# Performance work log

Hardware: AMD Instinct MI355X
Metric: run time of the kernel (lower is better)

Reference implementation:

```python
import jax, jax.numpy as jnp
import numpy as np

B, S, D, H = 4, 2048, 1024, 16
HD = D // H


def setup_inputs() -> dict:
    key = jax.random.key(0)
    ks = jax.random.split(key, 12)
    scale = 1.0 / np.sqrt(D)
    inp = {
        "query": jax.random.normal(ks[0], (B, S, D), jnp.float32),
        "key_": jax.random.normal(ks[1], (B, S, D), jnp.float32),
        "value": jax.random.normal(ks[2], (B, S, D), jnp.float32),
        "Wq": jax.random.normal(ks[3], (D, D), jnp.float32) * scale,
        "bq": jnp.zeros((D,), jnp.float32),
        "Wk": jax.random.normal(ks[4], (D, D), jnp.float32) * scale,
        "bk": jnp.zeros((D,), jnp.float32),
        "Wv": jax.random.normal(ks[5], (D, D), jnp.float32) * scale,
        "bv": jnp.zeros((D,), jnp.float32),
        "Wo": jax.random.normal(ks[6], (D, D), jnp.float32) * scale,
        "bo": jnp.zeros((D,), jnp.float32),
        # causal mask: 1 where attention allowed, 0 where masked (masked_fill(mask==0, -inf))
        "mask": jnp.tril(jnp.ones((S, S), jnp.int32))[None, None, :, :],
    }
    return inp


def reference(query, key_, value, Wq, bq, Wk, bk, Wv, bv, Wo, bo, mask):
    def split_heads(x):  # [B,S,D] -> [B,H,S,HD]
        return x.reshape(B, S, H, HD).transpose(0, 2, 1, 3)

    Q = split_heads(query @ Wq.T + bq)
    K = split_heads(key_ @ Wk.T + bk)
    V = split_heads(value @ Wv.T + bv)

    scores = jnp.einsum("bhqd,bhkd->bhqk", Q, K) / np.sqrt(HD).astype(np.float32)
    scores = jnp.where(mask == 0, -jnp.inf, scores)
    attn = jax.nn.softmax(scores, axis=-1)  # [B,H,S,S]
    out = jnp.einsum("bhqk,bhkd->bhqd", attn, V)  # [B,H,S,HD]
    concat = out.transpose(0, 2, 1, 3).reshape(B, S, D)
    return concat @ Wo.T + bo
```

## Files before the change

kernel.cpp:

```cpp
#include <hip/hip_runtime.h>
#include <hip/hip_bf16.h>
#include <math.h>

#define BB 4
#define SS 2048
#define DD 1024
#define HH 16
#define HD 64

#define NEG_BIG (-1e30f)


typedef short v8s __attribute__((ext_vector_type(8)));
typedef float v4f __attribute__((ext_vector_type(4)));

__device__ inline unsigned cvt_pk_bf16(float lo, float hi) {
    unsigned r;
    asm("v_cvt_pk_bf16_f32 %0, %1, %2" : "=v"(r) : "v"(lo), "v"(hi));
    return r;
}

__device__ inline short f2bf(float f) {
    return (short)cvt_pk_bf16(f, f);
}

__device__ inline v4f v4f_zero() {
    v4f z;
    z[0] = 0.f; z[1] = 0.f; z[2] = 0.f; z[3] = 0.f;
    return z;
}

__device__ inline v8s load8f(const float* p) {
    v4f a = *(const v4f*)p;
    v4f b = *(const v4f*)(p + 4);
    union { unsigned u[4]; v8s s; } x;
    x.u[0] = cvt_pk_bf16(a[0], a[1]);
    x.u[1] = cvt_pk_bf16(a[2], a[3]);
    x.u[2] = cvt_pk_bf16(b[0], b[1]);
    x.u[3] = cvt_pk_bf16(b[2], b[3]);
    return x.s;
}

template <int MODE>
__global__ __launch_bounds__(256) void gemm_bt_kernel(
    const void* __restrict__ Av, const float* __restrict__ Bm,
    const float* __restrict__ bias, void* __restrict__ Cv,
    int M, int N, int K) {
    __shared__ short sA[128 * 32];
    __shared__ short sB[128 * 32];

    const int tid = threadIdx.x;
    const int lane = tid & 63;
    const int wave = tid >> 6;
    const int quad = lane >> 4;
    const int l16 = lane & 15;
    const int wm = wave >> 1;
    const int wn = wave & 1;
    const int m0 = blockIdx.y * 128;
    const int n0 = blockIdx.x * 128;

    v4f acc[4][4];
#pragma unroll
    for (int i = 0; i < 4; i++)
#pragma unroll
        for (int j = 0; j < 4; j++) acc[i][j] = v4f_zero();

    for (int k0 = 0; k0 < K; k0 += 32) {
        __syncthreads();
#pragma unroll
        for (int p = 0; p < 2; p++) {
            int idx = (p * 256 + tid) * 8;
            int r = idx >> 5;
            int c = idx & 31;
            if (MODE == 3) {
                int m = m0 + r;
                int k = k0 + c;
                int b = m >> 11, s = m & 2047, h = k >> 6, d = k & 63;
                *(v8s*)&sA[idx] = *(const v8s*)&(
                    (const short*)Av)[(((size_t)(b * HH + h) * SS + s) << 6) + d];
            } else {
                *(v8s*)&sA[idx] =
                    load8f((const float*)Av + (size_t)(m0 + r) * K + k0 + c);
            }
            *(v8s*)&sB[idx] = load8f(Bm + (size_t)(n0 + r) * K + k0 + c);
        }
        __syncthreads();

        v8s af[4], bfr[4];
#pragma unroll
        for (int i = 0; i < 4; i++)
            af[i] = *(const v8s*)&sA[(wm * 64 + i * 16 + l16) * 32 + quad * 8];
#pragma unroll
        for (int j = 0; j < 4; j++)
            bfr[j] = *(const v8s*)&sB[(wn * 64 + j * 16 + l16) * 32 + quad * 8];
#pragma unroll
        for (int i = 0; i < 4; i++)
#pragma unroll
            for (int j = 0; j < 4; j++)
                acc[i][j] = __builtin_amdgcn_mfma_f32_16x16x32_bf16(
                    af[i], bfr[j], acc[i][j], 0, 0, 0);
    }

#pragma unroll
    for (int i = 0; i < 4; i++) {
#pragma unroll
        for (int j = 0; j < 4; j++) {
#pragma unroll
            for (int r = 0; r < 4; r++) {
                int ml = wm * 64 + i * 16 + quad * 4 + r;
                int nl = wn * 64 + j * 16 + l16;
                int m = m0 + ml;
                int n = n0 + nl;
                float v = acc[i][j][r];
                if (MODE == 0) {
                    v += bias[n];
                    int b = m >> 11, s = m & 2047, h = n >> 6, d = n & 63;
                    ((short*)Cv)[(((size_t)(b * HH + h) * SS + s) << 6) + d] =
                        f2bf(v);
                } else if (MODE == 1) {
                    v += bias[m];
                    int h = m >> 6, d = m & 63, b = n >> 11, s = n & 2047;
                    ((short*)Cv)[((size_t)(b * HH + h) * HD + d) * SS + s] =
                        f2bf(v);
                } else {
                    v += bias[n];
                    ((float*)Cv)[(size_t)m * N + n] = v;
                }
            }
        }
    }
}

__global__ __launch_bounds__(256) void attn_kernel(
    short* __restrict__ QO, const short* __restrict__ Kt,
    const short* __restrict__ Vt) {
    constexpr int LDR = 64 + 8;
    __shared__ short sK[64 * LDR];
    __shared__ short sV[64 * LDR];
    __shared__ short sP[4][16 * LDR];

    const int tid = threadIdx.x;
    const int lane = tid & 63;
    const int wave = tid >> 6;
    const int quad = lane >> 4;
    const int l16 = lane & 15;
    const int qt = (int)gridDim.x - 1 - (int)blockIdx.x;
    const int bh = blockIdx.y;

    short* Qh = QO + (size_t)bh * SS * HD;
    const short* Kh = Kt + (size_t)bh * SS * HD;
    const short* Vh = Vt + (size_t)bh * HD * SS;

    const int qrow = qt * 64 + wave * 16 + l16;
    v8s qf[2];
    qf[0] = *(const v8s*)&Qh[(size_t)qrow * HD + quad * 8];
    qf[1] = *(const v8s*)&Qh[(size_t)qrow * HD + 32 + quad * 8];

    v8s onesb;
#pragma unroll
    for (int i = 0; i < 8; i++) onesb[i] = (short)0x3F80;

    v4f o[4];
#pragma unroll
    for (int j = 0; j < 4; j++) o[j] = v4f_zero();
    v4f oSum = v4f_zero();
    float mOld[4];
#pragma unroll
    for (int r = 0; r < 4; r++) mOld[r] = NEG_BIG;

    const int qg_base = qt * 64 + wave * 16 + quad * 4;

    for (int kt = 0; kt <= qt; kt++) {
        __syncthreads();
#pragma unroll
        for (int p = 0; p < 2; p++) {
            int idx = (p * 256 + tid) * 8;
            int r = idx >> 6;
            int c = idx & 63;
            *(v8s*)&sK[r * LDR + c] =
                *(const v8s*)&Kh[(size_t)(kt * 64 + r) * HD + c];
            *(v8s*)&sV[r * LDR + c] =
                *(const v8s*)&Vh[(size_t)r * SS + kt * 64 + c];
        }
        __syncthreads();

        __builtin_amdgcn_s_setprio(1);
        v4f sc[4];
#pragma unroll
        for (int j = 0; j < 4; j++) {
            v8s b0 = *(const v8s*)&sK[(j * 16 + l16) * LDR + quad * 8];
            v8s b1 = *(const v8s*)&sK[(j * 16 + l16) * LDR + 32 + quad * 8];
            v4f t = __builtin_amdgcn_mfma_f32_16x16x32_bf16(qf[0], b0,
                                                            v4f_zero(), 0, 0, 0);
            sc[j] = __builtin_amdgcn_mfma_f32_16x16x32_bf16(qf[1], b1, t, 0, 0, 0);
        }
        __builtin_amdgcn_s_setprio(0);

        float x[4][4];
        const bool diag = (kt == qt);
#pragma unroll
        for (int j = 0; j < 4; j++) {
#pragma unroll
            for (int r = 0; r < 4; r++) {
                float v = sc[j][r] * 0.125f;
                if (diag) {
                    int kg = kt * 64 + j * 16 + l16;
                    int qg = qg_base + r;
                    if (kg > qg) v = NEG_BIG;
                }
                x[j][r] = v;
            }
        }

        float mNew[4], alpha[4];
#pragma unroll
        for (int r = 0; r < 4; r++) {
            float t = fmaxf(fmaxf(x[0][r], x[1][r]), fmaxf(x[2][r], x[3][r]));
#pragma unroll
            for (int off = 8; off >= 1; off >>= 1) t = fmaxf(t, __shfl_xor(t, off));
            mNew[r] = fmaxf(mOld[r], t);
            alpha[r] = __expf(mOld[r] - mNew[r]);
            mOld[r] = mNew[r];
        }

        short* Pw = sP[wave];
#pragma unroll
        for (int j = 0; j < 4; j++)
#pragma unroll
            for (int r = 0; r < 4; r++) {
                float p = __expf(x[j][r] - mNew[r]);
                Pw[(quad * 4 + r) * LDR + j * 16 + l16] = f2bf(p);
            }
#pragma unroll
        for (int j = 0; j < 4; j++)
#pragma unroll
            for (int r = 0; r < 4; r++) o[j][r] *= alpha[r];
#pragma unroll
        for (int r = 0; r < 4; r++) oSum[r] *= alpha[r];


        v8s pa0 = *(const v8s*)&Pw[l16 * LDR + quad * 8];
        v8s pa1 = *(const v8s*)&Pw[l16 * LDR + 32 + quad * 8];
        __builtin_amdgcn_s_setprio(1);
#pragma unroll
        for (int j = 0; j < 4; j++) {
            v8s v0 = *(const v8s*)&sV[(j * 16 + l16) * LDR + quad * 8];
            v8s v1 = *(const v8s*)&sV[(j * 16 + l16) * LDR + 32 + quad * 8];
            o[j] = __builtin_amdgcn_mfma_f32_16x16x32_bf16(pa0, v0, o[j], 0, 0, 0);
            o[j] = __builtin_amdgcn_mfma_f32_16x16x32_bf16(pa1, v1, o[j], 0, 0, 0);
        }
        oSum = __builtin_amdgcn_mfma_f32_16x16x32_bf16(pa0, onesb, oSum, 0, 0, 0);
        oSum = __builtin_amdgcn_mfma_f32_16x16x32_bf16(pa1, onesb, oSum, 0, 0, 0);
        __builtin_amdgcn_s_setprio(0);
    }

#pragma unroll
    for (int r = 0; r < 4; r++) {
        float inv = 1.f / oSum[r];
        int s = qg_base + r;
#pragma unroll
        for (int j = 0; j < 4; j++) {
            float v = o[j][r] * inv;
            Qh[(size_t)s * HD + j * 16 + l16] = f2bf(v);
        }
    }
}

extern "C" void kernel_launch(void* const* d_in, const int* in_sizes, int n_in,
                              void* d_out, int out_size, void* d_ws, size_t ws_size,
                              hipStream_t stream) {
    const float* query = (const float*)d_in[0];
    const float* key_ = (const float*)d_in[1];
    const float* value = (const float*)d_in[2];
    const float* Wq = (const float*)d_in[3];
    const float* bq = (const float*)d_in[4];
    const float* Wk = (const float*)d_in[5];
    const float* bk = (const float*)d_in[6];
    const float* Wv = (const float*)d_in[7];
    const float* bv = (const float*)d_in[8];
    const float* Wo = (const float*)d_in[9];
    const float* bo = (const float*)d_in[10];
    float* out = (float*)d_out;

    const size_t NE = (size_t)BB * SS * DD;

    short* qw = (short*)d_ws;
    short* kw = qw + NE;
    short* vw = (short*)d_out;

    dim3 blk(256);
    gemm_bt_kernel<0><<<dim3(8, 64), blk, 0, stream>>>(query, Wq, bq, qw, 8192, 1024, 1024);
    gemm_bt_kernel<0><<<dim3(8, 64), blk, 0, stream>>>(key_, Wk, bk, kw, 8192, 1024, 1024);
    gemm_bt_kernel<1><<<dim3(64, 8), blk, 0, stream>>>(Wv, value, bv, vw, 1024, 8192, 1024);
    attn_kernel<<<dim3(SS / 64, BB * HH), blk, 0, stream>>>(qw, kw, vw);
    gemm_bt_kernel<3><<<dim3(8, 64), blk, 0, stream>>>(qw, Wo, bo, out, 8192, 1024, 1024);
}
```

Before: 504.5 us.

## Pre-convert activations to bf16 and load GEMM tiles directly into LDS

Separate kernels convert the query, key and value activations to bf16 once, staging them in the output and workspace buffers. The projection GEMMs then stream that operand straight into shared memory with global_load_lds instead of loading fp32 and converting in registers. The Q and K projections are merged into one launch through blockIdx.z, and a block-index swizzle is added to improve L2 reuse. This removes repeated fp32 reads and conversions per tile, at the cost of extra conversion passes and the DRAM traffic they add.

```diff
diff --git a/kernel.cpp b/kernel.cpp
--- a/kernel.cpp
+++ b/kernel.cpp
@@ -41,11 +41,27 @@
     return x.s;
 }
 
+__device__ inline void gll16(const void* g, void* l) {
+    __builtin_amdgcn_global_load_lds(
+        (const __attribute__((address_space(1))) unsigned*)g,
+        (__attribute__((address_space(3))) unsigned*)l, 16, 0, 0);
+}
+
+__global__ __launch_bounds__(256) void conv_bf16_kernel(
+    const float* __restrict__ in, short* __restrict__ out, int n8) {
+    int i = blockIdx.x * 256 + threadIdx.x;
+    const int stride = gridDim.x * 256;
+    for (; i < n8; i += stride) {
+        *((v8s*)out + i) = load8f(in + (size_t)i * 8);
+    }
+}
+
 template <int MODE>
-__global__ __launch_bounds__(256) void gemm_bt_kernel(
-    const void* __restrict__ Av, const float* __restrict__ Bm,
-    const float* __restrict__ bias, void* __restrict__ Cv,
-    int M, int N, int K) {
+__global__ __launch_bounds__(256) void gemm_kernel(
+    const void* __restrict__ Pbig, const float* __restrict__ Psml,
+    const float* __restrict__ Pbias, void* __restrict__ PC,
+    const void* __restrict__ Pbig2, const float* __restrict__ Psml2,
+    const float* __restrict__ Pbias2, void* __restrict__ PC2) {
     __shared__ short sA[128 * 32];
     __shared__ short sB[128 * 32];
 
@@ -56,8 +72,44 @@
     const int l16 = lane & 15;
     const int wm = wave >> 1;
     const int wn = wave & 1;
-    const int m0 = blockIdx.y * 128;
-    const int n0 = blockIdx.x * 128;
+
+    const void* Big = Pbig;
+    const float* Sml = Psml;
+    const float* bias = Pbias;
+    void* Cv = PC;
+    if (MODE == 0 && blockIdx.z == 1) {
+        Big = Pbig2; Sml = Psml2; bias = Pbias2; Cv = PC2;
+    }
+
+    int bx = blockIdx.x, by = blockIdx.y;
+    if (MODE != 1) {
+        int b = bx + (by << 3);
+        int l = ((b & 7) << 6) + (b >> 3);
+        bx = l & 7;
+        by = l >> 3;
+    }
+    const int m0 = by * 128;
+    const int n0 = bx * 128;
+
+    short* sBig = (MODE == 1) ? sB : sA;
+    short* sSml = (MODE == 1) ? sA : sB;
+    const int grow = (wave << 5) + (lane >> 2);
+    const int gcol = (lane & 3) << 3;
+    const short* BigS = (const short*)Big;
+    size_t gbase0, gbase1;
+    if (MODE == 3) {
+        int ma = m0 + grow, mb = m0 + grow + 16;
+        gbase0 = ((size_t)((ma >> 11) * HH) * SS + (ma & 2047)) * HD;
+        gbase1 = ((size_t)((mb >> 11) * HH) * SS + (mb & 2047)) * HD;
+    } else {
+        int r0 = ((MODE == 1) ? n0 : m0) + grow;
+        gbase0 = (size_t)r0 * 1024 + gcol;
+        gbase1 = gbase0 + (size_t)16 * 1024;
+    }
+    short* ldst0 = sBig + (wave << 10);
+    short* ldst1 = ldst0 + 512;
+
+    const int sml_base = (MODE == 1) ? m0 : n0;
 
     v4f acc[4][4];
 #pragma unroll
@@ -65,24 +117,23 @@
 #pragma unroll
         for (int j = 0; j < 4; j++) acc[i][j] = v4f_zero();
 
-    for (int k0 = 0; k0 < K; k0 += 32) {
+    for (int k0 = 0; k0 < 1024; k0 += 32) {
         __syncthreads();
+        if (MODE == 3) {
+            size_t hoff = (size_t)(k0 >> 6) * (SS * HD) + (k0 & 63) + gcol;
+            gll16(BigS + gbase0 + hoff, ldst0);
+            gll16(BigS + gbase1 + hoff, ldst1);
+        } else {
+            gll16(BigS + gbase0 + k0, ldst0);
+            gll16(BigS + gbase1 + k0, ldst1);
+        }
 #pragma unroll
         for (int p = 0; p < 2; p++) {
-            int idx = (p * 256 + tid) * 8;
+            int idx = ((p << 8) + tid) << 3;
             int r = idx >> 5;
             int c = idx & 31;
-            if (MODE == 3) {
-                int m = m0 + r;
-                int k = k0 + c;
-                int b = m >> 11, s = m & 2047, h = k >> 6, d = k & 63;
-                *(v8s*)&sA[idx] = *(const v8s*)&(
-                    (const short*)Av)[(((size_t)(b * HH + h) * SS + s) << 6) + d];
-            } else {
-                *(v8s*)&sA[idx] =
-                    load8f((const float*)Av + (size_t)(m0 + r) * K + k0 + c);
-            }
-            *(v8s*)&sB[idx] = load8f(Bm + (size_t)(n0 + r) * K + k0 + c);
+            *(v8s*)&sSml[idx] =
+                load8f(Sml + (size_t)(sml_base + r) * 1024 + k0 + c);
         }
         __syncthreads();
 
@@ -124,7 +175,7 @@
                         f2bf(v);
                 } else {
                     v += bias[n];
-                    ((float*)Cv)[(size_t)m * N + n] = v;
+                    ((float*)Cv)[(size_t)m * 1024 + n] = v;
                 }
             }
         }
@@ -237,7 +288,6 @@
             for (int r = 0; r < 4; r++) o[j][r] *= alpha[r];
 #pragma unroll
         for (int r = 0; r < 4; r++) oSum[r] *= alpha[r];
-
 
         v8s pa0 = *(const v8s*)&Pw[l16 * LDR + quad * 8];
         v8s pa1 = *(const v8s*)&Pw[l16 * LDR + 32 + quad * 8];
@@ -284,14 +334,23 @@
 
     const size_t NE = (size_t)BB * SS * DD;
 
+    short* qx = (short*)d_out;
+    short* kx = (short*)d_out + NE;
+    short* vx = (short*)d_out + NE;
+    short* vw = (short*)d_out;
     short* qw = (short*)d_ws;
-    short* kw = qw + NE;
-    short* vw = (short*)d_out;
+    short* kw = (short*)d_ws + NE;
 
     dim3 blk(256);
-    gemm_bt_kernel<0><<<dim3(8, 64), blk, 0, stream>>>(query, Wq, bq, qw, 8192, 1024, 1024);
-    gemm_bt_kernel<0><<<dim3(8, 64), blk, 0, stream>>>(key_, Wk, bk, kw, 8192, 1024, 1024);
-    gemm_bt_kernel<1><<<dim3(64, 8), blk, 0, stream>>>(Wv, value, bv, vw, 1024, 8192, 1024);
+    const int n8 = (int)(NE / 8);
+    conv_bf16_kernel<<<dim3(2048), blk, 0, stream>>>(query, qx, n8);
+    conv_bf16_kernel<<<dim3(2048), blk, 0, stream>>>(key_, kx, n8);
+    gemm_kernel<0><<<dim3(8, 64, 2), blk, 0, stream>>>(
+        qx, Wq, bq, qw, kx, Wk, bk, kw);
+    conv_bf16_kernel<<<dim3(2048), blk, 0, stream>>>(value, vx, n8);
+    gemm_kernel<1><<<dim3(64, 8), blk, 0, stream>>>(
+        vx, Wv, bv, vw, nullptr, nullptr, nullptr, nullptr);
     attn_kernel<<<dim3(SS / 64, BB * HH), blk, 0, stream>>>(qw, kw, vw);
-    gemm_bt_kernel<3><<<dim3(8, 64), blk, 0, stream>>>(qw, Wo, bo, out, 8192, 1024, 1024);
-}
+    gemm_kernel<3><<<dim3(8, 64), blk, 0, stream>>>(
+        qw, Wo, bo, out, nullptr, nullptr, nullptr, nullptr);
+}
```

Result: no change. 508.7 us (+0.8%).
